# Kernel tuning notes

Hardware: AMD Instinct MI355X
Metric: run time of the kernel (lower is better)

## Reference

```python
import jax, jax.numpy as jnp
import numpy as np

IN, HID, OUT = 128, 128, 128
NU, NI = 100000, 50000
E = 500000
NEG_SLOPE = 0.01  # torch F.leaky_relu default


def graph_conv(x_src, W, b, src, dst, n_dst):
    """DGL GraphConv with norm='right': sum messages into dst, divide by in-degree, add bias."""
    h = x_src @ W                                   # [n_src, d_out] -- apply weight first
    agg = jax.ops.segment_sum(h[src], dst, num_segments=n_dst)  # irregular gather + scatter-add
    deg = jax.ops.segment_sum(jnp.ones(dst.shape, h.dtype), dst, num_segments=n_dst)
    return agg / jnp.clip(deg, 1.0)[:, None] + b


def setup_inputs() -> dict:
    key = jax.random.key(0)
    ks = jax.random.split(key, 16)
    inp = {
        "x_user": jax.random.normal(ks[0], (NU, IN), jnp.float32),
        "x_item": jax.random.normal(ks[1], (NI, IN), jnp.float32),
        "src_rates": jax.random.randint(ks[2], (E,), 0, NU),
        "dst_rates": jax.random.randint(ks[3], (E,), 0, NI),
        "src_rev": jax.random.randint(ks[4], (E,), 0, NI),
        "dst_rev": jax.random.randint(ks[5], (E,), 0, NU),
        # layer 1 per-relation GraphConv params
        "W1_rates": jax.random.normal(ks[6], (IN, HID), jnp.float32) / np.sqrt(IN),
        "b1_rates": jnp.zeros((HID,), jnp.float32),
        "W1_rev": jax.random.normal(ks[7], (IN, HID), jnp.float32) / np.sqrt(IN),
        "b1_rev": jnp.zeros((HID,), jnp.float32),
        # layer 2 per-relation GraphConv params
        "W2_rates": jax.random.normal(ks[8], (HID, OUT), jnp.float32) / np.sqrt(HID),
        "b2_rates": jnp.zeros((OUT,), jnp.float32),
        "W2_rev": jax.random.normal(ks[9], (HID, OUT), jnp.float32) / np.sqrt(HID),
        "b2_rev": jnp.zeros((OUT,), jnp.float32),
    }
    return inp


def reference(x_user, x_item, src_rates, dst_rates, src_rev, dst_rev,
              W1_rates, b1_rates, W1_rev, b1_rev,
              W2_rates, b2_rates, W2_rev, b2_rev):
    # layer 1: HeteroGraphConv(sum) -- each dst type receives from its one incoming relation
    h_item = graph_conv(x_user, W1_rates, b1_rates, src_rates, dst_rates, NI)
    h_user = graph_conv(x_item, W1_rev, b1_rev, src_rev, dst_rev, NU)
    h_item = jax.nn.leaky_relu(h_item, NEG_SLOPE)
    h_user = jax.nn.leaky_relu(h_user, NEG_SLOPE)
    # layer 2
    o_item = graph_conv(h_user, W2_rates, b2_rates, src_rates, dst_rates, NI)
    o_user = graph_conv(h_item, W2_rev, b2_rev, src_rev, dst_rev, NU)
    return (o_user, o_item)
```

## Files before the change

### kernel.cpp

```cpp
#include <hip/hip_runtime.h>
#include <cstdint>
#include <cstddef>

#define NUSER 100000
#define NITEM 50000
#define NTOT  150000
#define NEDGE 500000
#define NEG_SLOPE 0.01f
#define PADW 136

#define BROWS 512
#define BSHIFT 9
#define NBUCK ((NTOT + BROWS - 1) / BROWS)
#define GCAP  8192
#define EPB   2048
#define NBINB ((NEDGE + EPB - 1) / EPB)
#define NENT  (2 * EPB)

#define NTILE_I ((NITEM + 63) / 64)
#define NTILE_U ((NUSER + 63) / 64)
#define GBI 176
#define GBU 352

#define CVTB 2048

typedef __attribute__((ext_vector_type(8))) short bf16x8;
typedef __attribute__((ext_vector_type(4))) float f32x4;

__device__ __forceinline__ unsigned short f2bf(float f) {
    unsigned int u = __builtin_bit_cast(unsigned int, f);
    unsigned int r = u + 0x7fffu + ((u >> 16) & 1u);
    return (unsigned short)(r >> 16);
}
__device__ __forceinline__ float bf2f(unsigned int b) {
    unsigned int u = (b & 0xffffu) << 16;
    return __builtin_bit_cast(float, u);
}
__device__ __forceinline__ unsigned int pack2(float lo, float hi) {
    return (unsigned int)f2bf(lo) | ((unsigned int)f2bf(hi) << 16);
}


__global__ __launch_bounds__(512) void bin_edges(const int* __restrict__ src_rates, const int* __restrict__ dst_rates,
                                                 const int* __restrict__ src_rev,   const int* __restrict__ dst_rev,
                                                 int* __restrict__ bcnt, unsigned int* __restrict__ bbuf) {
    __shared__ int h[NBUCK];
    __shared__ int hs[NBUCK];
    __shared__ int hbase[NBUCK];
    __shared__ int hcur[NBUCK];
    __shared__ int bsc[512];
    __shared__ unsigned int stage[NENT];

    int t = threadIdx.x;
    int e0 = blockIdx.x * EPB;
    int n = NEDGE - e0; if (n > EPB) n = EPB;

    for (int i = t; i < NBUCK; i += 512) h[i] = 0;
    __syncthreads();

    for (int i = t; i < n; i += 512) {
        int e = e0 + i;
        atomicAdd(&h[dst_rates[e] >> BSHIFT], 1);
        atomicAdd(&h[(NITEM + dst_rev[e]) >> BSHIFT], 1);
    }
    __syncthreads();

    int v = (t < NBUCK) ? h[t] : 0;
    bsc[t] = v;
    __syncthreads();
    for (int off = 1; off < 512; off <<= 1) {
        int x = (t >= off) ? bsc[t - off] : 0;
        __syncthreads();
        bsc[t] += x;
        __syncthreads();
    }
    if (t < NBUCK) {
        int run = bsc[t] - v;
        hs[t] = run;
        hcur[t] = run;
        hbase[t] = (v > 0) ? atomicAdd(&bcnt[t], v) : 0;
    }
    __syncthreads();

    for (int i = t; i < n; i += 512) {
        int e = e0 + i;
        int r1 = dst_rates[e];
        int p1 = atomicAdd(&hcur[r1 >> BSHIFT], 1);
        if (p1 < NENT)
            stage[p1] = ((unsigned)(r1 & (BROWS - 1)) << 17) | (unsigned)src_rates[e];
        int r2 = NITEM + dst_rev[e];
        int p2 = atomicAdd(&hcur[r2 >> BSHIFT], 1);
        if (p2 < NENT)
            stage[p2] = ((unsigned)(r2 & (BROWS - 1)) << 17) | (unsigned)src_rev[e];
    }
    __syncthreads();

    int wid = t >> 6, lane = t & 63;
    for (int b = wid; b < NBUCK; b += 8) {
        int cnt = h[b];
        if (cnt > NENT) cnt = NENT;
        int gb = hbase[b];
        int sb = hs[b];
        for (int i = lane; i < cnt; i += 64) {
            int gpos = gb + i;
            if (gpos < GCAP) bbuf[(size_t)b * GCAP + gpos] = stage[sb + i];
        }
    }
}


__global__ __launch_bounds__(256) void build_csr(const int* __restrict__ bcnt,
                                                 const unsigned int* __restrict__ bbuf,
                                                 int* __restrict__ rp, int* __restrict__ csr) {
    __shared__ unsigned int ent[GCAP];
    __shared__ int h[BROWS], hs[BROWS];
    __shared__ int bsc[256];

    int bk = blockIdx.x, t = threadIdx.x;

    int ps = 0;
    for (int i = t; i < bk; i += 256) ps += bcnt[i];
    bsc[t] = ps;
    __syncthreads();
    for (int off = 128; off > 0; off >>= 1) {
        if (t < off) bsc[t] += bsc[t + off];
        __syncthreads();
    }
    int base = bsc[0];
    int n = bcnt[bk];
    if (n > GCAP) n = GCAP;
    __syncthreads();

    const unsigned int* src = bbuf + (size_t)bk * GCAP;
    for (int i = t; i < n; i += 256) ent[i] = src[i];
    h[t] = 0; h[t + 256] = 0;
    __syncthreads();

    for (int i = t; i < n; i += 256) atomicAdd(&h[ent[i] >> 17], 1);
    __syncthreads();

    int v0 = h[2 * t], v1 = h[2 * t + 1];
    int ls = v0 + v1;
    bsc[t] = ls;
    __syncthreads();
    for (int off = 1; off < 256; off <<= 1) {
        int x = (t >= off) ? bsc[t - off] : 0;
        __syncthreads();
        bsc[t] += x;
        __syncthreads();
    }
    int run = bsc[t] - ls;
    hs[2 * t] = run;
    hs[2 * t + 1] = run + v0;
    __syncthreads();

    for (int r = t; r < BROWS; r += 256) {
        int row = bk * BROWS + r;
        if (row < NTOT) rp[row] = base + hs[r];
        h[r] = 0;
    }
    if (bk == 0 && t == 0) rp[NTOT] = 2 * NEDGE;
    __syncthreads();

    for (int i = t; i < n; i += 256) {
        unsigned int ev = ent[i];
        int rl = (int)(ev >> 17);
        int pos = base + hs[rl] + atomicAdd(&h[rl], 1);
        csr[pos] = (int)(ev & 0x1FFFFu);
    }
}


__global__ void cvt_wprep(const float* __restrict__ xu, const float* __restrict__ xi,
                          unsigned short* __restrict__ dst,
                          const float* __restrict__ w0, const float* __restrict__ w1,
                          const float* __restrict__ w2, const float* __restrict__ w3,
                          unsigned short* __restrict__ wt) {
    if (blockIdx.x >= CVTB) {
        int widx = blockIdx.x - CVTB;
        const float* src = (widx == 0) ? w0 : (widx == 1) ? w1 : (widx == 2) ? w2 : w3;
        unsigned short* d = wt + (size_t)widx * 128 * PADW;
        for (int i = threadIdx.x; i < 16384; i += 256) {
            int k = i >> 7, c = i & 127;
            d[c * PADW + k] = f2bf(src[i]);
        }
        return;
    }
    const int n8u = NUSER * 128 / 8;
    const int n8  = (NUSER + NITEM) * 128 / 8;
    for (int i = blockIdx.x * blockDim.x + threadIdx.x; i < n8; i += CVTB * 256) {
        const float* s = (i < n8u) ? (xu + (size_t)i * 8) : (xi + (size_t)(i - n8u) * 8);
        float4 a = ((const float4*)s)[0];
        float4 b = ((const float4*)s)[1];
        uint4 o;
        o.x = pack2(a.x, a.y);
        o.y = pack2(a.z, a.w);
        o.z = pack2(b.x, b.y);
        o.w = pack2(b.z, b.w);
        ((uint4*)dst)[i] = o;
    }
}


__global__ __launch_bounds__(256) void aggregate_bf(const unsigned short* __restrict__ featA,
                                                    const unsigned short* __restrict__ featB,
                                                    const int* __restrict__ rp, const int* __restrict__ csr,
                                                    unsigned short* __restrict__ outb) {
    int row = blockIdx.x * 8 + (threadIdx.x >> 5);
    if (row >= NTOT) return;
    const unsigned short* feat = (row < NITEM) ? featA : featB;
    int l = threadIdx.x & 31;
    int sub = l >> 4, l16 = l & 15;
    int b = rp[row], e = rp[row + 1];
    float a0 = 0.f, a1 = 0.f, a2 = 0.f, a3 = 0.f, a4 = 0.f, a5 = 0.f, a6 = 0.f, a7 = 0.f;
    int j = b + sub;
    for (; j + 2 < e; j += 4) {
        int s0 = csr[j];
        int s1 = csr[j + 2];
        uint4 v0 = *((const uint4*)(feat + (size_t)s0 * 128) + l16);
        uint4 v1 = *((const uint4*)(feat + (size_t)s1 * 128) + l16);
        a0 += bf2f(v0.x); a1 += bf2f(v0.x >> 16);
        a2 += bf2f(v0.y); a3 += bf2f(v0.y >> 16);
        a4 += bf2f(v0.z); a5 += bf2f(v0.z >> 16);
        a6 += bf2f(v0.w); a7 += bf2f(v0.w >> 16);
        a0 += bf2f(v1.x); a1 += bf2f(v1.x >> 16);
        a2 += bf2f(v1.y); a3 += bf2f(v1.y >> 16);
        a4 += bf2f(v1.z); a5 += bf2f(v1.z >> 16);
        a6 += bf2f(v1.w); a7 += bf2f(v1.w >> 16);
    }
    if (j < e) {
        int s0 = csr[j];
        uint4 v0 = *((const uint4*)(feat + (size_t)s0 * 128) + l16);
        a0 += bf2f(v0.x); a1 += bf2f(v0.x >> 16);
        a2 += bf2f(v0.y); a3 += bf2f(v0.y >> 16);
        a4 += bf2f(v0.z); a5 += bf2f(v0.z >> 16);
        a6 += bf2f(v0.w); a7 += bf2f(v0.w >> 16);
    }
    a0 += __shfl_xor(a0, 16); a1 += __shfl_xor(a1, 16);
    a2 += __shfl_xor(a2, 16); a3 += __shfl_xor(a3, 16);
    a4 += __shfl_xor(a4, 16); a5 += __shfl_xor(a5, 16);
    a6 += __shfl_xor(a6, 16); a7 += __shfl_xor(a7, 16);
    if (sub == 0) {
        int deg = e - b;
        float inv = 1.0f / (float)(deg > 0 ? deg : 1);
        uint4 o;
        o.x = pack2(a0 * inv, a1 * inv);
        o.y = pack2(a2 * inv, a3 * inv);
        o.z = pack2(a4 * inv, a5 * inv);
        o.w = pack2(a6 * inv, a7 * inv);
        *((uint4*)(outb + (size_t)row * 128) + l16) = o;
    }
}


__global__ __launch_bounds__(256) void gemm_both(const unsigned short* __restrict__ in,
                                                 const unsigned short* __restrict__ wtI,
                                                 const unsigned short* __restrict__ wtU,
                                                 const float* __restrict__ bI,
                                                 const float* __restrict__ bU,
                                                 float* __restrict__ outFI, float* __restrict__ outFU,
                                                 unsigned short* __restrict__ outB,
                                                 int leaky) {
    __shared__ __attribute__((aligned(16))) unsigned short wl[128 * PADW];
    __shared__ __attribute__((aligned(16))) unsigned short xl[64 * PADW];
    int t = threadIdx.x;
    int bi = blockIdx.x;
    bool item = bi < GBI;
    int tbeg = item ? bi : bi - GBI;
    int nT   = item ? NTILE_I : NTILE_U;
    int gstr = item ? GBI : GBU;
    int rbeg = item ? 0 : NITEM;
    int Nend = item ? NITEM : NTOT;
    const unsigned short* wt = item ? wtI : wtU;
    const float* bias = item ? bI : bU;
    float* oF = item ? outFI : outFU;

    for (int i = t; i < 128 * PADW / 8; i += 256)
        ((uint4*)wl)[i] = ((const uint4*)wt)[i];

    int lane = t & 63, w = t >> 6;
    int l16 = lane & 15, kq = lane >> 4;
    int rowb = w * 16;

    float bv[8];
    #pragma unroll
    for (int t8 = 0; t8 < 8; ++t8) bv[t8] = bias[t8 * 16 + l16];

    for (int tt = tbeg; tt < nT; tt += gstr) {
        int row0 = rbeg + tt * 64;

        __syncthreads();
        for (int i = t; i < 1024; i += 256) {
            int r = i >> 4, c = i & 15;
            int row = row0 + r;
            uint4 v = make_uint4(0u, 0u, 0u, 0u);
            if (row < Nend) v = ((const uint4*)(in + (size_t)row * 128))[c];
            ((uint4*)xl)[r * (PADW / 8) + c] = v;
        }
        __syncthreads();

        f32x4 acc[8];
        #pragma unroll
        for (int i = 0; i < 8; ++i) acc[i] = (f32x4){0.f, 0.f, 0.f, 0.f};

        #pragma unroll
        for (int ks = 0; ks < 4; ++ks) {
            int ko = ks * 32 + kq * 8;
            bf16x8 af = *(const bf16x8*)&xl[(rowb + l16) * PADW + ko];
            #pragma unroll
            for (int t8 = 0; t8 < 8; ++t8) {
                bf16x8 bf = *(const bf16x8*)&wl[(t8 * 16 + l16) * PADW + ko];
                acc[t8] = __builtin_amdgcn_mfma_f32_16x16x32_bf16(af, bf, acc[t8], 0, 0, 0);
            }
        }

        if (outB == nullptr) {
            #pragma unroll
            for (int t8 = 0; t8 < 8; ++t8) {
                #pragma unroll
                for (int j = 0; j < 4; ++j) {
                    int row = row0 + rowb + kq * 4 + j;
                    if (row < Nend) {
                        float v = acc[t8][j] + bv[t8];
                        if (leaky) v = v > 0.f ? v : NEG_SLOPE * v;
                        oF[(size_t)(row - rbeg) * 128 + t8 * 16 + l16] = v;
                    }
                }
            }
        } else {
            #pragma unroll
            for (int t8 = 0; t8 < 8; ++t8) {
                #pragma unroll
                for (int j = 0; j < 4; ++j) {
                    float v = acc[t8][j] + bv[t8];
                    if (leaky) v = v > 0.f ? v : NEG_SLOPE * v;
                    xl[(rowb + kq * 4 + j) * PADW + t8 * 16 + l16] = f2bf(v);
                }
            }
            __syncthreads();
            for (int i = t; i < 1024; i += 256) {
                int r = i >> 4, c = i & 15;
                int row = row0 + r;
                if (row < Nend)
                    ((uint4*)(outB + (size_t)row * 128))[c] = ((uint4*)xl)[r * (PADW / 8) + c];
            }
        }
    }
}


extern "C" void kernel_launch(void* const* d_in, const int* in_sizes, int n_in,
                              void* d_out, int out_size, void* d_ws, size_t ws_size,
                              hipStream_t stream) {
    const float* x_user    = (const float*)d_in[0];
    const float* x_item    = (const float*)d_in[1];
    const int*   src_rates = (const int*)d_in[2];
    const int*   dst_rates = (const int*)d_in[3];
    const int*   src_rev   = (const int*)d_in[4];
    const int*   dst_rev   = (const int*)d_in[5];
    const float* W1_rates  = (const float*)d_in[6];
    const float* b1_rates  = (const float*)d_in[7];
    const float* W1_rev    = (const float*)d_in[8];
    const float* b1_rev    = (const float*)d_in[9];
    const float* W2_rates  = (const float*)d_in[10];
    const float* b2_rates  = (const float*)d_in[11];
    const float* W2_rev    = (const float*)d_in[12];
    const float* b2_rev    = (const float*)d_in[13];

    float* out    = (float*)d_out;
    float* o_user = out;
    float* o_item = out + (size_t)NUSER * 128;

    char* ws = (char*)d_ws;
    size_t off = 0;
    auto carve = [&](size_t bytes) -> void* {
        void* p = ws + off;
        off = (off + bytes + 255) & ~(size_t)255;
        return p;
    };
    unsigned short* A = (unsigned short*)carve((size_t)NTOT * 128 * 2);
    unsigned short* B = (unsigned short*)carve((size_t)NTOT * 128 * 2);
    int* rp    = (int*)carve((size_t)(NTOT + 1) * 4);
    int* bcnt  = (int*)carve((size_t)NBUCK * 4);
    int* csr   = (int*)carve((size_t)(2 * NEDGE) * 4);
    unsigned short* wtAll = (unsigned short*)carve((size_t)4 * 128 * PADW * 2);
    unsigned short* Wt1_rates = wtAll;
    unsigned short* Wt1_rev   = wtAll + 1 * (size_t)128 * PADW;
    unsigned short* Wt2_rates = wtAll + 2 * (size_t)128 * PADW;
    unsigned short* Wt2_rev   = wtAll + 3 * (size_t)128 * PADW;

    unsigned int* bbuf = (unsigned int*)B;

    unsigned short* xu_bf = A;
    unsigned short* xi_bf = A + (size_t)NUSER * 128;
    unsigned short* h_item = A;
    unsigned short* h_user = A + (size_t)NITEM * 128;

    hipMemsetAsync(bcnt, 0, (size_t)NBUCK * 4, stream);
    bin_edges<<<NBINB, 512, 0, stream>>>(src_rates, dst_rates, src_rev, dst_rev, bcnt, bbuf);
    build_csr<<<NBUCK, 256, 0, stream>>>(bcnt, bbuf, rp, csr);

    cvt_wprep<<<CVTB + 4, 256, 0, stream>>>(x_user, x_item, A,
                                            W1_rates, W1_rev, W2_rates, W2_rev, wtAll);

    int nbAgg = (NTOT + 7) / 8;

    aggregate_bf<<<nbAgg, 256, 0, stream>>>(xu_bf, xi_bf, rp, csr, B);
    gemm_both<<<GBI + GBU, 256, 0, stream>>>(B, Wt1_rates, Wt1_rev, b1_rates, b1_rev,
                                             nullptr, nullptr, A, 1);

    aggregate_bf<<<nbAgg, 256, 0, stream>>>(h_user, h_item, rp, csr, B);
    gemm_both<<<GBI + GBU, 256, 0, stream>>>(B, Wt2_rates, Wt2_rev, b2_rates, b2_rev,
                                             o_item, o_user, nullptr, 0);
}
```

Measured before the change: 208.4 us.

## Reorder to transform-then-aggregate and fuse input conversion into GEMM

Switches each layer from aggregate-then-GEMM to GEMM-then-aggregate, matching the reference order. The bias, leaky ReLU and fp32 output stores move into the aggregation epilogue. The first GEMM now reads the fp32 inputs directly and converts them to bf16 while loading tiles, which removes the separate conversion kernel and its extra pass over the input features. Weight prep becomes its own small kernel launched before CSR construction. The rounding order changes, since the GEMM output is rounded to bf16 before summation, which may shift numerical error slightly.

```diff
diff --git a/kernel.cpp b/kernel.cpp
--- a/kernel.cpp
+++ b/kernel.cpp
@@ -16,13 +16,6 @@
 #define EPB   2048
 #define NBINB ((NEDGE + EPB - 1) / EPB)
 #define NENT  (2 * EPB)
-
-#define NTILE_I ((NITEM + 63) / 64)
-#define NTILE_U ((NUSER + 63) / 64)
-#define GBI 176
-#define GBU 352
-
-#define CVTB 2048
 
 typedef __attribute__((ext_vector_type(8))) short bf16x8;
 typedef __attribute__((ext_vector_type(4))) float f32x4;
@@ -171,44 +164,28 @@
 }
 
 
-__global__ void cvt_wprep(const float* __restrict__ xu, const float* __restrict__ xi,
-                          unsigned short* __restrict__ dst,
-                          const float* __restrict__ w0, const float* __restrict__ w1,
-                          const float* __restrict__ w2, const float* __restrict__ w3,
-                          unsigned short* __restrict__ wt) {
-    if (blockIdx.x >= CVTB) {
-        int widx = blockIdx.x - CVTB;
-        const float* src = (widx == 0) ? w0 : (widx == 1) ? w1 : (widx == 2) ? w2 : w3;
-        unsigned short* d = wt + (size_t)widx * 128 * PADW;
-        for (int i = threadIdx.x; i < 16384; i += 256) {
-            int k = i >> 7, c = i & 127;
-            d[c * PADW + k] = f2bf(src[i]);
-        }
-        return;
-    }
-    const int n8u = NUSER * 128 / 8;
-    const int n8  = (NUSER + NITEM) * 128 / 8;
-    for (int i = blockIdx.x * blockDim.x + threadIdx.x; i < n8; i += CVTB * 256) {
-        const float* s = (i < n8u) ? (xu + (size_t)i * 8) : (xi + (size_t)(i - n8u) * 8);
-        float4 a = ((const float4*)s)[0];
-        float4 b = ((const float4*)s)[1];
-        uint4 o;
-        o.x = pack2(a.x, a.y);
-        o.y = pack2(a.z, a.w);
-        o.z = pack2(b.x, b.y);
-        o.w = pack2(b.z, b.w);
-        ((uint4*)dst)[i] = o;
-    }
-}
-
-
-__global__ __launch_bounds__(256) void aggregate_bf(const unsigned short* __restrict__ featA,
+__global__ void wprep(const float* __restrict__ w0, const float* __restrict__ w1,
+                      const float* __restrict__ w2, const float* __restrict__ w3,
+                      unsigned short* __restrict__ wt) {
+    const float* src = (blockIdx.x == 0) ? w0 : (blockIdx.x == 1) ? w1 : (blockIdx.x == 2) ? w2 : w3;
+    unsigned short* dst = wt + (size_t)blockIdx.x * 128 * PADW;
+    for (int i = threadIdx.x; i < 16384; i += 256) {
+        int k = i >> 7, c = i & 127;
+        dst[c * PADW + k] = f2bf(src[i]);
+    }
+}
+
+
+__global__ __launch_bounds__(256) void aggregate_ep(const unsigned short* __restrict__ featA,
                                                     const unsigned short* __restrict__ featB,
                                                     const int* __restrict__ rp, const int* __restrict__ csr,
-                                                    unsigned short* __restrict__ outb) {
+                                                    const float* __restrict__ bI, const float* __restrict__ bU,
+                                                    unsigned short* __restrict__ outb,
+                                                    float* __restrict__ outI, float* __restrict__ outU) {
     int row = blockIdx.x * 8 + (threadIdx.x >> 5);
     if (row >= NTOT) return;
-    const unsigned short* feat = (row < NITEM) ? featA : featB;
+    bool item = row < NITEM;
+    const unsigned short* feat = item ? featA : featB;
     int l = threadIdx.x & 31;
     int sub = l >> 4, l16 = l & 15;
     int b = rp[row], e = rp[row + 1];
@@ -243,37 +220,58 @@
     if (sub == 0) {
         int deg = e - b;
         float inv = 1.0f / (float)(deg > 0 ? deg : 1);
-        uint4 o;
-        o.x = pack2(a0 * inv, a1 * inv);
-        o.y = pack2(a2 * inv, a3 * inv);
-        o.z = pack2(a4 * inv, a5 * inv);
-        o.w = pack2(a6 * inv, a7 * inv);
-        *((uint4*)(outb + (size_t)row * 128) + l16) = o;
-    }
-}
-
-
-__global__ __launch_bounds__(256) void gemm_both(const unsigned short* __restrict__ in,
-                                                 const unsigned short* __restrict__ wtI,
-                                                 const unsigned short* __restrict__ wtU,
-                                                 const float* __restrict__ bI,
-                                                 const float* __restrict__ bU,
-                                                 float* __restrict__ outFI, float* __restrict__ outFU,
+        const float* bias = item ? bI : bU;
+        float4 bv0 = ((const float4*)bias)[l16 * 2];
+        float4 bv1 = ((const float4*)bias)[l16 * 2 + 1];
+        float r0 = a0 * inv + bv0.x, r1 = a1 * inv + bv0.y;
+        float r2 = a2 * inv + bv0.z, r3 = a3 * inv + bv0.w;
+        float r4 = a4 * inv + bv1.x, r5 = a5 * inv + bv1.y;
+        float r6 = a6 * inv + bv1.z, r7 = a7 * inv + bv1.w;
+        if (outI) {
+            float* o = item ? (outI + (size_t)row * 128) : (outU + (size_t)(row - NITEM) * 128);
+            float4 o0, o1;
+            o0.x = r0; o0.y = r1; o0.z = r2; o0.w = r3;
+            o1.x = r4; o1.y = r5; o1.z = r6; o1.w = r7;
+            ((float4*)o)[l16 * 2]     = o0;
+            ((float4*)o)[l16 * 2 + 1] = o1;
+        } else {
+            r0 = r0 > 0.f ? r0 : NEG_SLOPE * r0;
+            r1 = r1 > 0.f ? r1 : NEG_SLOPE * r1;
+            r2 = r2 > 0.f ? r2 : NEG_SLOPE * r2;
+            r3 = r3 > 0.f ? r3 : NEG_SLOPE * r3;
+            r4 = r4 > 0.f ? r4 : NEG_SLOPE * r4;
+            r5 = r5 > 0.f ? r5 : NEG_SLOPE * r5;
+            r6 = r6 > 0.f ? r6 : NEG_SLOPE * r6;
+            r7 = r7 > 0.f ? r7 : NEG_SLOPE * r7;
+            uint4 o;
+            o.x = pack2(r0, r1);
+            o.y = pack2(r2, r3);
+            o.z = pack2(r4, r5);
+            o.w = pack2(r6, r7);
+            *((uint4*)(outb + (size_t)row * 128) + l16) = o;
+        }
+    }
+}
+
+
+__global__ __launch_bounds__(256) void gemm_both(const float* __restrict__ xfU, const float* __restrict__ xfI,
+                                                 const unsigned short* __restrict__ inB,
+                                                 const unsigned short* __restrict__ wt0,
+                                                 const unsigned short* __restrict__ wt1,
                                                  unsigned short* __restrict__ outB,
-                                                 int leaky) {
+                                                 int nR0, int g0, int g1) {
     __shared__ __attribute__((aligned(16))) unsigned short wl[128 * PADW];
     __shared__ __attribute__((aligned(16))) unsigned short xl[64 * PADW];
     int t = threadIdx.x;
     int bi = blockIdx.x;
-    bool item = bi < GBI;
-    int tbeg = item ? bi : bi - GBI;
-    int nT   = item ? NTILE_I : NTILE_U;
-    int gstr = item ? GBI : GBU;
-    int rbeg = item ? 0 : NITEM;
-    int Nend = item ? NITEM : NTOT;
-    const unsigned short* wt = item ? wtI : wtU;
-    const float* bias = item ? bI : bU;
-    float* oF = item ? outFI : outFU;
+    bool reg0 = bi < g0;
+    int tbeg = reg0 ? bi : bi - g0;
+    int gstr = reg0 ? g0 : g1;
+    int rbeg = reg0 ? 0 : nR0;
+    int rcnt = reg0 ? nR0 : NTOT - nR0;
+    int Nend = rbeg + rcnt;
+    int nT = (rcnt + 63) / 64;
+    const unsigned short* wt = reg0 ? wt0 : wt1;
 
     for (int i = t; i < 128 * PADW / 8; i += 256)
         ((uint4*)wl)[i] = ((const uint4*)wt)[i];
@@ -282,20 +280,35 @@
     int l16 = lane & 15, kq = lane >> 4;
     int rowb = w * 16;
 
-    float bv[8];
-    #pragma unroll
-    for (int t8 = 0; t8 < 8; ++t8) bv[t8] = bias[t8 * 16 + l16];
-
     for (int tt = tbeg; tt < nT; tt += gstr) {
         int row0 = rbeg + tt * 64;
 
         __syncthreads();
-        for (int i = t; i < 1024; i += 256) {
-            int r = i >> 4, c = i & 15;
-            int row = row0 + r;
-            uint4 v = make_uint4(0u, 0u, 0u, 0u);
-            if (row < Nend) v = ((const uint4*)(in + (size_t)row * 128))[c];
-            ((uint4*)xl)[r * (PADW / 8) + c] = v;
+        if (xfU) {
+            for (int i = t; i < 1024; i += 256) {
+                int r = i >> 4, c = i & 15;
+                int row = row0 + r;
+                uint4 v = make_uint4(0u, 0u, 0u, 0u);
+                if (row < Nend) {
+                    const float* s = (row < NUSER) ? (xfU + (size_t)row * 128 + c * 8)
+                                                   : (xfI + (size_t)(row - NUSER) * 128 + c * 8);
+                    float4 a = ((const float4*)s)[0];
+                    float4 b = ((const float4*)s)[1];
+                    v.x = pack2(a.x, a.y);
+                    v.y = pack2(a.z, a.w);
+                    v.z = pack2(b.x, b.y);
+                    v.w = pack2(b.z, b.w);
+                }
+                ((uint4*)xl)[r * (PADW / 8) + c] = v;
+            }
+        } else {
+            for (int i = t; i < 1024; i += 256) {
+                int r = i >> 4, c = i & 15;
+                int row = row0 + r;
+                uint4 v = make_uint4(0u, 0u, 0u, 0u);
+                if (row < Nend) v = ((const uint4*)(inB + (size_t)row * 128))[c];
+                ((uint4*)xl)[r * (PADW / 8) + c] = v;
+            }
         }
         __syncthreads();
 
@@ -314,36 +327,18 @@
             }
         }
 
-        if (outB == nullptr) {
+        #pragma unroll
+        for (int t8 = 0; t8 < 8; ++t8) {
             #pragma unroll
-            for (int t8 = 0; t8 < 8; ++t8) {
-                #pragma unroll
-                for (int j = 0; j < 4; ++j) {
-                    int row = row0 + rowb + kq * 4 + j;
-                    if (row < Nend) {
-                        float v = acc[t8][j] + bv[t8];
-                        if (leaky) v = v > 0.f ? v : NEG_SLOPE * v;
-                        oF[(size_t)(row - rbeg) * 128 + t8 * 16 + l16] = v;
-                    }
-                }
-            }
-        } else {
-            #pragma unroll
-            for (int t8 = 0; t8 < 8; ++t8) {
-                #pragma unroll
-                for (int j = 0; j < 4; ++j) {
-                    float v = acc[t8][j] + bv[t8];
-                    if (leaky) v = v > 0.f ? v : NEG_SLOPE * v;
-                    xl[(rowb + kq * 4 + j) * PADW + t8 * 16 + l16] = f2bf(v);
-                }
-            }
-            __syncthreads();
-            for (int i = t; i < 1024; i += 256) {
-                int r = i >> 4, c = i & 15;
-                int row = row0 + r;
-                if (row < Nend)
-                    ((uint4*)(outB + (size_t)row * 128))[c] = ((uint4*)xl)[r * (PADW / 8) + c];
-            }
+            for (int j = 0; j < 4; ++j)
+                xl[(rowb + kq * 4 + j) * PADW + t8 * 16 + l16] = f2bf(acc[t8][j]);
+        }
+        __syncthreads();
+        for (int i = t; i < 1024; i += 256) {
+            int r = i >> 4, c = i & 15;
+            int row = row0 + r;
+            if (row < Nend)
+                ((uint4*)(outB + (size_t)row * 128))[c] = ((uint4*)xl)[r * (PADW / 8) + c];
         }
     }
 }
@@ -391,25 +386,20 @@
 
     unsigned int* bbuf = (unsigned int*)B;
 
-    unsigned short* xu_bf = A;
-    unsigned short* xi_bf = A + (size_t)NUSER * 128;
-    unsigned short* h_item = A;
-    unsigned short* h_user = A + (size_t)NITEM * 128;
-
     hipMemsetAsync(bcnt, 0, (size_t)NBUCK * 4, stream);
+    wprep<<<4, 256, 0, stream>>>(W1_rates, W1_rev, W2_rates, W2_rev, wtAll);
     bin_edges<<<NBINB, 512, 0, stream>>>(src_rates, dst_rates, src_rev, dst_rev, bcnt, bbuf);
     build_csr<<<NBUCK, 256, 0, stream>>>(bcnt, bbuf, rp, csr);
 
-    cvt_wprep<<<CVTB + 4, 256, 0, stream>>>(x_user, x_item, A,
-                                            W1_rates, W1_rev, W2_rates, W2_rev, wtAll);
-
     int nbAgg = (NTOT + 7) / 8;
 
-    aggregate_bf<<<nbAgg, 256, 0, stream>>>(xu_bf, xi_bf, rp, csr, B);
-    gemm_both<<<GBI + GBU, 256, 0, stream>>>(B, Wt1_rates, Wt1_rev, b1_rates, b1_rev,
-                                             nullptr, nullptr, A, 1);
-
-    aggregate_bf<<<nbAgg, 256, 0, stream>>>(h_user, h_item, rp, csr, B);
-    gemm_both<<<GBI + GBU, 256, 0, stream>>>(B, Wt2_rates, Wt2_rev, b2_rates, b2_rev,
-                                             o_item, o_user, nullptr, 0);
-}
+    gemm_both<<<528, 256, 0, stream>>>(x_user, x_item, nullptr,
+                                       Wt1_rates, Wt1_rev, A, NUSER, 352, 176);
+    aggregate_ep<<<nbAgg, 256, 0, stream>>>(A, A + (size_t)NUSER * 128, rp, csr,
+                                            b1_rates, b1_rev, B, nullptr, nullptr);
+
+    gemm_both<<<528, 256, 0, stream>>>(nullptr, nullptr, B,
+                                       Wt2_rev, Wt2_rates, A, NITEM, 176, 352);
+    aggregate_ep<<<nbAgg, 256, 0, stream>>>(A + (size_t)NITEM * 128, A, rp, csr,
+                                            b2_rates, b2_rev, nullptr, o_item, o_user);
+}
```

Result: faster. 201.3 us (-3.4%).
